# Kernel tuning notes

Hardware: AMD Instinct MI355X
Metric: run time of the kernel (lower is better)

The kernel has to match this reference:

```python
import jax, jax.numpy as jnp
import numpy as np

B, C, H, W = 4, 128, 64, 64


def setup_inputs() -> dict:
    key = jax.random.key(0)
    ks = jax.random.split(key, 7)
    s = 1.0 / np.sqrt(C)
    return {
        "x": jax.random.normal(ks[0], (B, C, H, W), dtype=jnp.float32),
        "Wq": jax.random.normal(ks[1], (C, C), dtype=jnp.float32) * s,
        "bq": jnp.zeros((C,), dtype=jnp.float32),
        "Wk": jax.random.normal(ks[2], (C, C), dtype=jnp.float32) * s,
        "bk": jnp.zeros((C,), dtype=jnp.float32),
        "Wv": jax.random.normal(ks[3], (C, C), dtype=jnp.float32) * s,
        "bv": jnp.zeros((C,), dtype=jnp.float32),
    }


def reference(x, Wq, bq, Wk, bk, Wv, bv):
    b, c, h, w = x.shape
    n = h * w
    scale = c ** (-0.5)
    # tokens: [B, N, C]
    xt = x.reshape(b, c, n).transpose(0, 2, 1)
    # 1x1 convs == per-token channel GEMMs (out[c'] = sum_c W[c',c] x[c] + b[c'])
    q = jnp.einsum("bnc,dc->bnd", xt, Wq) + bq  # [B, N, C]
    k = jnp.einsum("bnc,dc->bnd", xt, Wk) + bk  # [B, N, C]
    v = jnp.einsum("bnc,dc->bnd", xt, Wv) + bv  # [B, N, C]
    scores = jnp.einsum("bic,bjc->bij", q, k) * scale  # [B, N, N]
    attn = jax.nn.softmax(scores, axis=-1)
    out = jnp.einsum("bij,bjc->bic", attn, v)  # [B, N, C]
    return out.transpose(0, 2, 1).reshape(b, c, h, w)
```

## Files before the change

kernel.cpp:

```cpp
#include <hip/hip_runtime.h>
#include <hip/hip_bf16.h>


#define BATCH 4
#define CH    128
#define NTOK  4096
#define TK    64
#define SCALE 0.08838834764831845f
#define LOG2E 1.4426950408889634f
#define MFIX  16.0f
#define PSTR  72

typedef __attribute__((ext_vector_type(8)))  short short8;
typedef __attribute__((ext_vector_type(4)))  float f32x4;
typedef __attribute__((ext_vector_type(16))) float f32x16;

static __device__ __forceinline__ unsigned short f2bf(float f) {
    __hip_bfloat16 h = (__hip_bfloat16)f;
    return *(const unsigned short*)&h;
}

__global__ __launch_bounds__(256) void convert_w_kernel(
    const float* __restrict__ Wq, const float* __restrict__ Wk,
    const float* __restrict__ Wv, unsigned short* __restrict__ wb)
{
    const int idx = (blockIdx.x * 256 + threadIdx.x) * 4;
    const float* srcs[3] = {Wq, Wk, Wv};
    #pragma unroll
    for (int m = 0; m < 3; ++m) {
        float4 v = *(const float4*)(srcs[m] + idx);
        unsigned short o[4] = {f2bf(v.x), f2bf(v.y), f2bf(v.z), f2bf(v.w)};
        *(uint2*)(wb + (size_t)m * CH * CH + idx) = *(const uint2*)o;
    }
}

__global__ __launch_bounds__(256) void proj_mfma_kernel(
    const float* __restrict__ x,
    const unsigned short* __restrict__ wqb, const unsigned short* __restrict__ wkb,
    const unsigned short* __restrict__ wvb,
    const float* __restrict__ bq, const float* __restrict__ bk,
    const float* __restrict__ bv,
    unsigned short* __restrict__ q_ws, unsigned short* __restrict__ k_ws,
    unsigned short* __restrict__ vt_ws)
{
    __shared__ __align__(16) unsigned short XsT[64 * CH];

    const int t    = threadIdx.x;
    const int w    = t >> 6;
    const int lane = t & 63;
    const int quad = lane >> 4;
    const int c16  = lane & 15;
    const int n0   = blockIdx.x * 64;
    const int b    = blockIdx.y;
    const float* xb = x + (size_t)b * CH * NTOK;

    {
        const int tok = lane;
        #pragma unroll
        for (int cc = 0; cc < 4; ++cc) {
            const int cb = 32 * w + 8 * cc;
            unsigned short tmp[8];
            #pragma unroll
            for (int j = 0; j < 8; ++j)
                tmp[j] = f2bf(xb[(size_t)(cb + j) * NTOK + n0 + tok]);
            const int phys = ((cb >> 3) ^ (tok & 15));
            *(short8*)&XsT[tok * CH + phys * 8] = *(const short8*)tmp;
        }
    }
    __syncthreads();

    short8 xa[4];
    #pragma unroll
    for (int ks = 0; ks < 4; ++ks)
        xa[ks] = *(const short8*)&XsT[(16 * w + c16) * CH + (((4 * ks + quad) ^ c16) << 3)];

    #pragma unroll
    for (int nt = 0; nt < 8; ++nt) {
        f32x4 aq = (f32x4){0.f, 0.f, 0.f, 0.f};
        f32x4 ak = (f32x4){0.f, 0.f, 0.f, 0.f};
        const unsigned short* wqr = wqb + (16 * nt + c16) * CH;
        const unsigned short* wkr = wkb + (16 * nt + c16) * CH;
        #pragma unroll
        for (int ks = 0; ks < 4; ++ks) {
            const short8 bqf = *(const short8*)(wqr + 32 * ks + 8 * quad);
            const short8 bkf = *(const short8*)(wkr + 32 * ks + 8 * quad);
            aq = __builtin_amdgcn_mfma_f32_16x16x32_bf16(xa[ks], bqf, aq, 0, 0, 0);
            ak = __builtin_amdgcn_mfma_f32_16x16x32_bf16(xa[ks], bkf, ak, 0, 0, 0);
        }
        const float bqv = bq[16 * nt + c16];
        const float bkv = bk[16 * nt + c16];
        #pragma unroll
        for (int r = 0; r < 4; ++r) {
            const int n = n0 + 16 * w + quad * 4 + r;
            const size_t o = ((size_t)b * NTOK + n) * CH + 16 * nt + c16;
            q_ws[o] = f2bf((aq[r] + bqv) * (SCALE * LOG2E));
            k_ws[o] = f2bf(ak[r] + bkv);
        }
    }

    short8 wva[2][4];
    float  bvv[2][4];
    #pragma unroll
    for (int mt = 0; mt < 2; ++mt) {
        const int crow16 = 16 * (2 * w + mt);
        #pragma unroll
        for (int ks = 0; ks < 4; ++ks)
            wva[mt][ks] = *(const short8*)&wvb[(crow16 + c16) * CH + 32 * ks + 8 * quad];
        #pragma unroll
        for (int r = 0; r < 4; ++r)
            bvv[mt][r] = bv[crow16 + quad * 4 + r];
    }
    #pragma unroll
    for (int nt = 0; nt < 4; ++nt) {
        short8 xbf[4];
        #pragma unroll
        for (int ks = 0; ks < 4; ++ks)
            xbf[ks] = *(const short8*)&XsT[(16 * nt + c16) * CH + (((4 * ks + quad) ^ c16) << 3)];
        #pragma unroll
        for (int mt = 0; mt < 2; ++mt) {
            f32x4 acc = (f32x4){0.f, 0.f, 0.f, 0.f};
            #pragma unroll
            for (int ks = 0; ks < 4; ++ks)
                acc = __builtin_amdgcn_mfma_f32_16x16x32_bf16(wva[mt][ks], xbf[ks], acc, 0, 0, 0);
            #pragma unroll
            for (int r = 0; r < 4; ++r) {
                const int crow = 16 * (2 * w + mt) + quad * 4 + r;
                vt_ws[((size_t)b * CH + crow) * NTOK + n0 + 16 * nt + c16] =
                    f2bf(acc[r] + bvv[mt][r]);
            }
        }
    }
}

template <int SPLIT>
__global__ __launch_bounds__(256, 2) void flash_attn_mfma(
    const unsigned short* __restrict__ q_ws,
    const unsigned short* __restrict__ k_ws,
    const unsigned short* __restrict__ vt_ws,
    float* __restrict__ out,
    float* __restrict__ Op, float* __restrict__ l_p)
{
    __shared__ __align__(16) unsigned short KsU[TK * CH];
    __shared__ __align__(16) unsigned short VtU[CH * TK];
    __shared__ __align__(16) unsigned short PlU[4 * 32 * PSTR];

    const int t    = threadIdx.x;
    const int w    = t >> 6;
    const int lane = t & 63;
    const int half = lane >> 5;
    const int l32  = lane & 31;
    const int jc   = blockIdx.y;
    const int b    = blockIdx.z;
    const int n0   = blockIdx.x * 128;
    const int jbeg = jc * (NTOK / SPLIT);
    const int jend = jbeg + (NTOK / SPLIT);

    short8 qa[8];
    {
        const unsigned short* qrow = q_ws + ((size_t)b * NTOK + n0 + 32 * w + l32) * CH;
        #pragma unroll
        for (int ks = 0; ks < 8; ++ks)
            qa[ks] = *(const short8*)(qrow + ks * 16 + half * 8);
    }

    f32x16 Oa[4];
    #pragma unroll
    for (int ct = 0; ct < 4; ++ct) Oa[ct] = (f32x16)(0.0f);
    f32x16 La = (f32x16)(0.0f);

    const unsigned short* kg = k_ws  + (size_t)b * NTOK * CH;
    const unsigned short* vg = vt_ws + (size_t)b * CH * NTOK;
    const short8 ones8 = (short8)(short)0x3F80;
    unsigned short* Pw = &PlU[w * 32 * PSTR];

    for (int j0 = jbeg; j0 < jend; j0 += TK) {
        __syncthreads();

        {
            const int rl = lane >> 4, u = lane & 15;
            #pragma unroll
            for (int ci = 0; ci < 4; ++ci) {
                const int row = 16 * w + 4 * ci + rl;
                const int g   = u ^ (row & 15);
                const unsigned short* src = kg + (size_t)(j0 + row) * CH + g * 8;
                __builtin_amdgcn_global_load_lds(
                    (const __attribute__((address_space(1))) void*)src,
                    (__attribute__((address_space(3))) void*)&KsU[(16 * w + 4 * ci) * CH],
                    16, 0, 0);
            }
        }
        {
            const int cl = lane >> 3, u = lane & 7;
            #pragma unroll
            for (int ci = 0; ci < 4; ++ci) {
                const int c = 32 * w + 8 * ci + cl;
                const int g = u ^ (c & 7);
                const unsigned short* src = vg + (size_t)c * NTOK + j0 + g * 8;
                __builtin_amdgcn_global_load_lds(
                    (const __attribute__((address_space(1))) void*)src,
                    (__attribute__((address_space(3))) void*)&VtU[(32 * w + 8 * ci) * TK],
                    16, 0, 0);
            }
        }
        __syncthreads();

        f32x16 s0 = (f32x16)(-MFIX);
        f32x16 s1 = (f32x16)(-MFIX);
        #pragma unroll
        for (int ks = 0; ks < 8; ++ks) {
            const int ph = (2 * ks + half) ^ (l32 & 15);
            const short8 kf0 = *(const short8*)&KsU[l32 * CH + ph * 8];
            const short8 kf1 = *(const short8*)&KsU[(32 + l32) * CH + ph * 8];
            s0 = __builtin_amdgcn_mfma_f32_32x32x16_bf16(qa[ks], kf0, s0, 0, 0, 0);
            s1 = __builtin_amdgcn_mfma_f32_32x32x16_bf16(qa[ks], kf1, s1, 0, 0, 0);
        }

        #pragma unroll
        for (int reg = 0; reg < 16; ++reg) {
            const int row = (reg & 3) + 8 * (reg >> 2) + 4 * half;
            Pw[row * PSTR + l32]      = f2bf(exp2f(s0[reg]));
            Pw[row * PSTR + 32 + l32] = f2bf(exp2f(s1[reg]));
        }
        __threadfence_block();

        #pragma unroll
        for (int ks2 = 0; ks2 < 4; ++ks2) {
            const short8 pa = *(const short8*)&Pw[l32 * PSTR + ks2 * 16 + half * 8];
            #pragma unroll
            for (int ct = 0; ct < 4; ++ct) {
                const int ch = ct * 32 + l32;
                const int ph = (2 * ks2 + half) ^ (ch & 7);
                const short8 vf = *(const short8*)&VtU[ch * TK + ph * 8];
                Oa[ct] = __builtin_amdgcn_mfma_f32_32x32x16_bf16(pa, vf, Oa[ct], 0, 0, 0);
            }
            La = __builtin_amdgcn_mfma_f32_32x32x16_bf16(pa, ones8, La, 0, 0, 0);
        }
    }

    if constexpr (SPLIT == 1) {
        #pragma unroll
        for (int reg = 0; reg < 16; ++reg) {
            const int row = (reg & 3) + 8 * (reg >> 2) + 4 * half;
            const int n = n0 + 32 * w + row;
            const float inv = 1.0f / La[reg];
            #pragma unroll
            for (int ct = 0; ct < 4; ++ct)
                out[((size_t)b * CH + ct * 32 + l32) * NTOK + n] = Oa[ct][reg] * inv;
        }
    } else {
        const size_t chunk = (size_t)(b * SPLIT + jc);
        #pragma unroll
        for (int reg = 0; reg < 16; ++reg) {
            const int row = (reg & 3) + 8 * (reg >> 2) + 4 * half;
            const int n = n0 + 32 * w + row;
            const size_t base = (chunk * NTOK + n) * CH;
            #pragma unroll
            for (int ct = 0; ct < 4; ++ct)
                Op[base + ct * 32 + l32] = Oa[ct][reg];
            if (l32 == 0) l_p[chunk * NTOK + n] = La[reg];
        }
    }
}

template <int SPLIT>
__global__ __launch_bounds__(256) void combine_kernel(
    const float* __restrict__ Op, const float* __restrict__ l_p,
    float* __restrict__ out)
{
    const int t  = threadIdx.x;
    const int cg = t & 31;
    const int r8 = t >> 5;
    const int n0 = blockIdx.x * 64;
    const int b  = blockIdx.y;

    for (int it = 0; it < 8; ++it) {
        const int n = n0 + it * 8 + r8;
        float den = 0.f;
        float4 acc = make_float4(0.f, 0.f, 0.f, 0.f);
        #pragma unroll
        for (int j = 0; j < SPLIT; ++j) {
            const size_t chunk = (size_t)(b * SPLIT + j);
            den += l_p[chunk * NTOK + n];
            const float4 o = *(const float4*)&Op[(chunk * NTOK + n) * CH + cg * 4];
            acc.x += o.x; acc.y += o.y; acc.z += o.z; acc.w += o.w;
        }
        const float inv = 1.0f / den;
        out[((size_t)b * CH + cg * 4 + 0) * NTOK + n] = acc.x * inv;
        out[((size_t)b * CH + cg * 4 + 1) * NTOK + n] = acc.y * inv;
        out[((size_t)b * CH + cg * 4 + 2) * NTOK + n] = acc.z * inv;
        out[((size_t)b * CH + cg * 4 + 3) * NTOK + n] = acc.w * inv;
    }
}

extern "C" void kernel_launch(void* const* d_in, const int* in_sizes, int n_in,
                              void* d_out, int out_size, void* d_ws, size_t ws_size,
                              hipStream_t stream) {
    const float* x  = (const float*)d_in[0];
    const float* Wq = (const float*)d_in[1];
    const float* bq = (const float*)d_in[2];
    const float* Wk = (const float*)d_in[3];
    const float* bk = (const float*)d_in[4];
    const float* Wv = (const float*)d_in[5];
    const float* bv = (const float*)d_in[6];
    float* out = (float*)d_out;

    const size_t QKV = (size_t)BATCH * NTOK * CH;
    unsigned short* q_ws  = (unsigned short*)d_ws;
    unsigned short* k_ws  = q_ws + QKV;
    unsigned short* vt_ws = k_ws + QKV;
    unsigned short* wb    = vt_ws + QKV;
    float* Op = (float*)(wb + 3 * CH * CH);

    const size_t baseBytes = 3 * QKV * 2 + 3 * CH * CH * 2;
    auto needBytes = [&](size_t S) {
        return baseBytes + S * BATCH * NTOK * (size_t)(CH * 4 + 4);
    };

    convert_w_kernel<<<CH * CH / (256 * 4), 256, 0, stream>>>(Wq, Wk, Wv, wb);

    dim3 gp(NTOK / 64, BATCH);
    proj_mfma_kernel<<<gp, 256, 0, stream>>>(x, wb, wb + CH * CH, wb + 2 * CH * CH,
                                             bq, bk, bv, q_ws, k_ws, vt_ws);

    if (ws_size >= needBytes(8)) {
        float* l_p = Op + (size_t)8 * BATCH * NTOK * CH;
        dim3 ga(NTOK / 128, 8, BATCH);
        flash_attn_mfma<8><<<ga, 256, 0, stream>>>(q_ws, k_ws, vt_ws, out, Op, l_p);
        dim3 gc(NTOK / 64, BATCH);
        combine_kernel<8><<<gc, 256, 0, stream>>>(Op, l_p, out);
    } else if (ws_size >= needBytes(4)) {
        float* l_p = Op + (size_t)4 * BATCH * NTOK * CH;
        dim3 ga(NTOK / 128, 4, BATCH);
        flash_attn_mfma<4><<<ga, 256, 0, stream>>>(q_ws, k_ws, vt_ws, out, Op, l_p);
        dim3 gc(NTOK / 64, BATCH);
        combine_kernel<4><<<gc, 256, 0, stream>>>(Op, l_p, out);
    } else {
        dim3 ga(NTOK / 128, 1, BATCH);
        flash_attn_mfma<1><<<ga, 256, 0, stream>>>(q_ws, k_ws, vt_ws, out,
                                                   nullptr, nullptr);
    }
}
```

Measured before the change: 146.6 us.

## Double-buffer K/V tiles, keep P in registers, retile attention waves, coalesce combine

The attention kernel now double-buffers the K and V tiles in LDS and prefetches the next tile with a partial vmcnt wait, so loads overlap compute. It computes transposed scores, so P is packed to bf16 with v_cvt_pk_bf16 and permlane32_swap entirely in registers. This removes the LDS round trip for P and the ones-MFMA row sum, which is replaced by scalar sums plus a shuffle. Waves are retiled as 2 query-halves x 2 channel-halves, the partial-output layout becomes channel-major so the combine kernel does fully vectorized float4 reads and writes, and the split count drops from 8 to 4. Doubling LDS may lower occupancy, and the smaller split reduces grid parallelism.

```diff
diff --git a/kernel.cpp b/kernel.cpp
--- a/kernel.cpp
+++ b/kernel.cpp
@@ -9,7 +9,6 @@
 #define SCALE 0.08838834764831845f
 #define LOG2E 1.4426950408889634f
 #define MFIX  16.0f
-#define PSTR  72
 
 typedef __attribute__((ext_vector_type(8)))  short short8;
 typedef __attribute__((ext_vector_type(4)))  float f32x4;
@@ -18,6 +17,12 @@
 static __device__ __forceinline__ unsigned short f2bf(float f) {
     __hip_bfloat16 h = (__hip_bfloat16)f;
     return *(const unsigned short*)&h;
+}
+
+static __device__ __forceinline__ unsigned cvt_pk_bf16(float lo, float hi) {
+    unsigned r;
+    asm("v_cvt_pk_bf16_f32 %0, %1, %2" : "=v"(r) : "v"(lo), "v"(hi));
+    return r;
 }
 
 __global__ __launch_bounds__(256) void convert_w_kernel(
@@ -140,124 +145,182 @@
     float* __restrict__ out,
     float* __restrict__ Op, float* __restrict__ l_p)
 {
-    __shared__ __align__(16) unsigned short KsU[TK * CH];
-    __shared__ __align__(16) unsigned short VtU[CH * TK];
-    __shared__ __align__(16) unsigned short PlU[4 * 32 * PSTR];
+    __shared__ __align__(16) unsigned short KsU[2][TK * CH];
+    __shared__ __align__(16) unsigned short VtU[2][CH * TK];
 
     const int t    = threadIdx.x;
     const int w    = t >> 6;
     const int lane = t & 63;
     const int half = lane >> 5;
     const int l32  = lane & 31;
+    const int qhw  = w >> 1;
+    const int chw  = w & 1;
     const int jc   = blockIdx.y;
     const int b    = blockIdx.z;
     const int n0   = blockIdx.x * 128;
     const int jbeg = jc * (NTOK / SPLIT);
-    const int jend = jbeg + (NTOK / SPLIT);
-
-    short8 qa[8];
-    {
-        const unsigned short* qrow = q_ws + ((size_t)b * NTOK + n0 + 32 * w + l32) * CH;
-        #pragma unroll
-        for (int ks = 0; ks < 8; ++ks)
-            qa[ks] = *(const short8*)(qrow + ks * 16 + half * 8);
-    }
-
-    f32x16 Oa[4];
-    #pragma unroll
-    for (int ct = 0; ct < 4; ++ct) Oa[ct] = (f32x16)(0.0f);
-    f32x16 La = (f32x16)(0.0f);
+    constexpr int NT = (NTOK / SPLIT) / TK;
 
     const unsigned short* kg = k_ws  + (size_t)b * NTOK * CH;
     const unsigned short* vg = vt_ws + (size_t)b * CH * NTOK;
-    const short8 ones8 = (short8)(short)0x3F80;
-    unsigned short* Pw = &PlU[w * 32 * PSTR];
-
-    for (int j0 = jbeg; j0 < jend; j0 += TK) {
-        __syncthreads();
-
-        {
-            const int rl = lane >> 4, u = lane & 15;
-            #pragma unroll
-            for (int ci = 0; ci < 4; ++ci) {
-                const int row = 16 * w + 4 * ci + rl;
-                const int g   = u ^ (row & 15);
-                const unsigned short* src = kg + (size_t)(j0 + row) * CH + g * 8;
-                __builtin_amdgcn_global_load_lds(
-                    (const __attribute__((address_space(1))) void*)src,
-                    (__attribute__((address_space(3))) void*)&KsU[(16 * w + 4 * ci) * CH],
-                    16, 0, 0);
-            }
-        }
-        {
-            const int cl = lane >> 3, u = lane & 7;
-            #pragma unroll
-            for (int ci = 0; ci < 4; ++ci) {
-                const int c = 32 * w + 8 * ci + cl;
-                const int g = u ^ (c & 7);
-                const unsigned short* src = vg + (size_t)c * NTOK + j0 + g * 8;
-                __builtin_amdgcn_global_load_lds(
-                    (const __attribute__((address_space(1))) void*)src,
-                    (__attribute__((address_space(3))) void*)&VtU[(32 * w + 8 * ci) * TK],
-                    16, 0, 0);
-            }
-        }
-        __syncthreads();
-
-        f32x16 s0 = (f32x16)(-MFIX);
-        f32x16 s1 = (f32x16)(-MFIX);
+
+    short8 qa[2][8];
+    #pragma unroll
+    for (int qs = 0; qs < 2; ++qs) {
+        const unsigned short* qrow =
+            q_ws + ((size_t)b * NTOK + n0 + 64 * qhw + 32 * qs + l32) * CH;
+        #pragma unroll
+        for (int ks = 0; ks < 8; ++ks)
+            qa[qs][ks] = *(const short8*)(qrow + ks * 16 + half * 8);
+    }
+
+    f32x16 Oa[2][2];
+    #pragma unroll
+    for (int qs = 0; qs < 2; ++qs)
+        #pragma unroll
+        for (int ct = 0; ct < 2; ++ct) Oa[qs][ct] = (f32x16)(0.0f);
+    float lsum[2] = {0.f, 0.f};
+
+    const int krl = lane >> 4, ku = lane & 15;
+    const int vcl = lane >> 3, vu = lane & 7;
+
+    auto STAGE = [&](int buf, int jj) {
+        #pragma unroll
+        for (int ci = 0; ci < 4; ++ci) {
+            const int row = 16 * w + 4 * ci + krl;
+            const int g   = ku ^ (row & 15);
+            const unsigned short* src = kg + (size_t)(jj + row) * CH + g * 8;
+            __builtin_amdgcn_global_load_lds(
+                (const __attribute__((address_space(1))) void*)src,
+                (__attribute__((address_space(3))) void*)&KsU[buf][(16 * w + 4 * ci) * CH],
+                16, 0, 0);
+        }
+        #pragma unroll
+        for (int ci = 0; ci < 4; ++ci) {
+            const int c = 32 * w + 8 * ci + vcl;
+            const int g = vu ^ (c & 7);
+            const unsigned short* src = vg + (size_t)c * NTOK + jj + g * 8;
+            __builtin_amdgcn_global_load_lds(
+                (const __attribute__((address_space(1))) void*)src,
+                (__attribute__((address_space(3))) void*)&VtU[buf][(32 * w + 8 * ci) * TK],
+                16, 0, 0);
+        }
+    };
+
+    STAGE(0, jbeg);
+
+    int j0 = jbeg;
+    for (int tt = 0; tt < NT; ++tt, j0 += TK) {
+        const int cur = tt & 1;
+        if (tt + 1 < NT) {
+            STAGE(cur ^ 1, j0 + TK);
+            asm volatile("s_waitcnt vmcnt(8)" ::: "memory");
+        } else {
+            asm volatile("s_waitcnt vmcnt(0)" ::: "memory");
+        }
+        __builtin_amdgcn_sched_barrier(0);
+        __builtin_amdgcn_s_barrier();
+        __builtin_amdgcn_sched_barrier(0);
+
+        const unsigned short* Kc = &KsU[cur][0];
+        const unsigned short* Vc = &VtU[cur][0];
+
+        f32x16 s[2][2];
+        #pragma unroll
+        for (int qs = 0; qs < 2; ++qs)
+            #pragma unroll
+            for (int kt = 0; kt < 2; ++kt) s[qs][kt] = (f32x16)(-MFIX);
+
         #pragma unroll
         for (int ks = 0; ks < 8; ++ks) {
             const int ph = (2 * ks + half) ^ (l32 & 15);
-            const short8 kf0 = *(const short8*)&KsU[l32 * CH + ph * 8];
-            const short8 kf1 = *(const short8*)&KsU[(32 + l32) * CH + ph * 8];
-            s0 = __builtin_amdgcn_mfma_f32_32x32x16_bf16(qa[ks], kf0, s0, 0, 0, 0);
-            s1 = __builtin_amdgcn_mfma_f32_32x32x16_bf16(qa[ks], kf1, s1, 0, 0, 0);
-        }
-
-        #pragma unroll
-        for (int reg = 0; reg < 16; ++reg) {
-            const int row = (reg & 3) + 8 * (reg >> 2) + 4 * half;
-            Pw[row * PSTR + l32]      = f2bf(exp2f(s0[reg]));
-            Pw[row * PSTR + 32 + l32] = f2bf(exp2f(s1[reg]));
-        }
-        __threadfence_block();
+            const short8 kf0 = *(const short8*)&Kc[l32 * CH + ph * 8];
+            const short8 kf1 = *(const short8*)&Kc[(32 + l32) * CH + ph * 8];
+            s[0][0] = __builtin_amdgcn_mfma_f32_32x32x16_bf16(kf0, qa[0][ks], s[0][0], 0, 0, 0);
+            s[1][0] = __builtin_amdgcn_mfma_f32_32x32x16_bf16(kf0, qa[1][ks], s[1][0], 0, 0, 0);
+            s[0][1] = __builtin_amdgcn_mfma_f32_32x32x16_bf16(kf1, qa[0][ks], s[0][1], 0, 0, 0);
+            s[1][1] = __builtin_amdgcn_mfma_f32_32x32x16_bf16(kf1, qa[1][ks], s[1][1], 0, 0, 0);
+        }
+
+        short8 pb[2][4];
+        #pragma unroll
+        for (int qs = 0; qs < 2; ++qs) {
+            #pragma unroll
+            for (int kt = 0; kt < 2; ++kt) {
+                float p[16];
+                #pragma unroll
+                for (int r = 0; r < 16; ++r) p[r] = exp2f(s[qs][kt][r]);
+                float a0 = 0.f, a1 = 0.f, a2 = 0.f, a3 = 0.f;
+                #pragma unroll
+                for (int r = 0; r < 4; ++r) {
+                    a0 += p[r]; a1 += p[4 + r]; a2 += p[8 + r]; a3 += p[12 + r];
+                }
+                lsum[qs] += (a0 + a1) + (a2 + a3);
+                unsigned wd[8];
+                #pragma unroll
+                for (int i = 0; i < 8; ++i) wd[i] = cvt_pk_bf16(p[2 * i], p[2 * i + 1]);
+                auto r02 = __builtin_amdgcn_permlane32_swap(wd[0], wd[2], false, false);
+                auto r13 = __builtin_amdgcn_permlane32_swap(wd[1], wd[3], false, false);
+                auto r46 = __builtin_amdgcn_permlane32_swap(wd[4], wd[6], false, false);
+                auto r57 = __builtin_amdgcn_permlane32_swap(wd[5], wd[7], false, false);
+                union { unsigned u[4]; short8 s8; } f0, f1;
+                f0.u[0] = r02[0]; f0.u[1] = r13[0]; f0.u[2] = r02[1]; f0.u[3] = r13[1];
+                f1.u[0] = r46[0]; f1.u[1] = r57[0]; f1.u[2] = r46[1]; f1.u[3] = r57[1];
+                pb[qs][2 * kt + 0] = f0.s8;
+                pb[qs][2 * kt + 1] = f1.s8;
+            }
+        }
 
         #pragma unroll
         for (int ks2 = 0; ks2 < 4; ++ks2) {
-            const short8 pa = *(const short8*)&Pw[l32 * PSTR + ks2 * 16 + half * 8];
-            #pragma unroll
-            for (int ct = 0; ct < 4; ++ct) {
-                const int ch = ct * 32 + l32;
+            #pragma unroll
+            for (int ct = 0; ct < 2; ++ct) {
+                const int ch = 64 * chw + 32 * ct + l32;
                 const int ph = (2 * ks2 + half) ^ (ch & 7);
-                const short8 vf = *(const short8*)&VtU[ch * TK + ph * 8];
-                Oa[ct] = __builtin_amdgcn_mfma_f32_32x32x16_bf16(pa, vf, Oa[ct], 0, 0, 0);
-            }
-            La = __builtin_amdgcn_mfma_f32_32x32x16_bf16(pa, ones8, La, 0, 0, 0);
-        }
-    }
+                const short8 vf = *(const short8*)&Vc[ch * TK + ph * 8];
+                Oa[0][ct] = __builtin_amdgcn_mfma_f32_32x32x16_bf16(vf, pb[0][ks2], Oa[0][ct], 0, 0, 0);
+                Oa[1][ct] = __builtin_amdgcn_mfma_f32_32x32x16_bf16(vf, pb[1][ks2], Oa[1][ct], 0, 0, 0);
+            }
+        }
+        __builtin_amdgcn_sched_barrier(0);
+        __builtin_amdgcn_s_barrier();
+        __builtin_amdgcn_sched_barrier(0);
+    }
+
+    float lt[2];
+    #pragma unroll
+    for (int qs = 0; qs < 2; ++qs)
+        lt[qs] = lsum[qs] + __shfl_xor(lsum[qs], 32);
 
     if constexpr (SPLIT == 1) {
         #pragma unroll
-        for (int reg = 0; reg < 16; ++reg) {
-            const int row = (reg & 3) + 8 * (reg >> 2) + 4 * half;
-            const int n = n0 + 32 * w + row;
-            const float inv = 1.0f / La[reg];
-            #pragma unroll
-            for (int ct = 0; ct < 4; ++ct)
-                out[((size_t)b * CH + ct * 32 + l32) * NTOK + n] = Oa[ct][reg] * inv;
+        for (int qs = 0; qs < 2; ++qs) {
+            const float inv = 1.0f / lt[qs];
+            const int n = n0 + 64 * qhw + 32 * qs + l32;
+            #pragma unroll
+            for (int ct = 0; ct < 2; ++ct) {
+                #pragma unroll
+                for (int r = 0; r < 16; ++r) {
+                    const int c = 64 * chw + 32 * ct + (r & 3) + 8 * (r >> 2) + 4 * half;
+                    out[((size_t)b * CH + c) * NTOK + n] = Oa[qs][ct][r] * inv;
+                }
+            }
         }
     } else {
         const size_t chunk = (size_t)(b * SPLIT + jc);
         #pragma unroll
-        for (int reg = 0; reg < 16; ++reg) {
-            const int row = (reg & 3) + 8 * (reg >> 2) + 4 * half;
-            const int n = n0 + 32 * w + row;
-            const size_t base = (chunk * NTOK + n) * CH;
-            #pragma unroll
-            for (int ct = 0; ct < 4; ++ct)
-                Op[base + ct * 32 + l32] = Oa[ct][reg];
-            if (l32 == 0) l_p[chunk * NTOK + n] = La[reg];
+        for (int qs = 0; qs < 2; ++qs) {
+            const int n = n0 + 64 * qhw + 32 * qs + l32;
+            #pragma unroll
+            for (int ct = 0; ct < 2; ++ct) {
+                #pragma unroll
+                for (int r = 0; r < 16; ++r) {
+                    const int c = 64 * chw + 32 * ct + (r & 3) + 8 * (r >> 2) + 4 * half;
+                    Op[(chunk * CH + c) * NTOK + n] = Oa[qs][ct][r];
+                }
+            }
+            if (chw == 0 && half == 0)
+                l_p[chunk * NTOK + n] = lt[qs];
         }
     }
 }
@@ -267,29 +330,24 @@
     const float* __restrict__ Op, const float* __restrict__ l_p,
     float* __restrict__ out)
 {
-    const int t  = threadIdx.x;
-    const int cg = t & 31;
-    const int r8 = t >> 5;
-    const int n0 = blockIdx.x * 64;
-    const int b  = blockIdx.y;
-
-    for (int it = 0; it < 8; ++it) {
-        const int n = n0 + it * 8 + r8;
-        float den = 0.f;
-        float4 acc = make_float4(0.f, 0.f, 0.f, 0.f);
-        #pragma unroll
-        for (int j = 0; j < SPLIT; ++j) {
-            const size_t chunk = (size_t)(b * SPLIT + j);
-            den += l_p[chunk * NTOK + n];
-            const float4 o = *(const float4*)&Op[(chunk * NTOK + n) * CH + cg * 4];
-            acc.x += o.x; acc.y += o.y; acc.z += o.z; acc.w += o.w;
-        }
-        const float inv = 1.0f / den;
-        out[((size_t)b * CH + cg * 4 + 0) * NTOK + n] = acc.x * inv;
-        out[((size_t)b * CH + cg * 4 + 1) * NTOK + n] = acc.y * inv;
-        out[((size_t)b * CH + cg * 4 + 2) * NTOK + n] = acc.z * inv;
-        out[((size_t)b * CH + cg * 4 + 3) * NTOK + n] = acc.w * inv;
-    }
+    const int b = blockIdx.y;
+    const size_t idx = ((size_t)blockIdx.x * 256 + threadIdx.x) * 4;
+    const int c = (int)(idx >> 12);
+    const int n = (int)(idx & (NTOK - 1));
+    float4 acc = make_float4(0.f, 0.f, 0.f, 0.f);
+    float4 den = make_float4(0.f, 0.f, 0.f, 0.f);
+    #pragma unroll
+    for (int j = 0; j < SPLIT; ++j) {
+        const size_t chunk = (size_t)(b * SPLIT + j);
+        const float4 o = *(const float4*)&Op[(chunk * CH + c) * NTOK + n];
+        const float4 d = *(const float4*)&l_p[chunk * NTOK + n];
+        acc.x += o.x; acc.y += o.y; acc.z += o.z; acc.w += o.w;
+        den.x += d.x; den.y += d.y; den.z += d.z; den.w += d.w;
+    }
+    float4 r;
+    r.x = acc.x / den.x; r.y = acc.y / den.y;
+    r.z = acc.z / den.z; r.w = acc.w / den.w;
+    *(float4*)&out[((size_t)b * CH * NTOK) + idx] = r;
 }
 
 extern "C" void kernel_launch(void* const* d_in, const int* in_sizes, int n_in,
@@ -322,18 +380,17 @@
     proj_mfma_kernel<<<gp, 256, 0, stream>>>(x, wb, wb + CH * CH, wb + 2 * CH * CH,
                                              bq, bk, bv, q_ws, k_ws, vt_ws);
 
-    if (ws_size >= needBytes(8)) {
-        float* l_p = Op + (size_t)8 * BATCH * NTOK * CH;
-        dim3 ga(NTOK / 128, 8, BATCH);
-        flash_attn_mfma<8><<<ga, 256, 0, stream>>>(q_ws, k_ws, vt_ws, out, Op, l_p);
-        dim3 gc(NTOK / 64, BATCH);
-        combine_kernel<8><<<gc, 256, 0, stream>>>(Op, l_p, out);
-    } else if (ws_size >= needBytes(4)) {
+    dim3 gc(CH * NTOK / 1024, BATCH);
+    if (ws_size >= needBytes(4)) {
         float* l_p = Op + (size_t)4 * BATCH * NTOK * CH;
         dim3 ga(NTOK / 128, 4, BATCH);
         flash_attn_mfma<4><<<ga, 256, 0, stream>>>(q_ws, k_ws, vt_ws, out, Op, l_p);
-        dim3 gc(NTOK / 64, BATCH);
         combine_kernel<4><<<gc, 256, 0, stream>>>(Op, l_p, out);
+    } else if (ws_size >= needBytes(2)) {
+        float* l_p = Op + (size_t)2 * BATCH * NTOK * CH;
+        dim3 ga(NTOK / 128, 2, BATCH);
+        flash_attn_mfma<2><<<ga, 256, 0, stream>>>(q_ws, k_ws, vt_ws, out, Op, l_p);
+        combine_kernel<2><<<gc, 256, 0, stream>>>(Op, l_p, out);
     } else {
         dim3 ga(NTOK / 128, 1, BATCH);
         flash_attn_mfma<1><<<ga, 256, 0, stream>>>(q_ws, k_ws, vt_ws, out,
```

After: 174.6 us. +19.1%, slower.
